# Kernel optimization log

Hardware: AMD Instinct MI355X
Metric: run time of the kernel (lower is better)

Reference implementation:

```python
import jax, jax.numpy as jnp
import numpy as np

H = 24        # attn.heads (Flux)
ENC = 512     # encoder (text) token count, hard-coded in the source via emb[:512]
EPS = 1e-6    # RMSNorm eps


def _rms(x, w):
    # RMSNorm over head_dim (Flux norm_q / norm_k)
    return x * jax.lax.rsqrt(jnp.mean(x * x, axis=-1, keepdims=True) + EPS) * w


def _rope(x, cos, sin):
    # diffusers apply_rotary_emb, use_real=True, unbind_dim=-1
    xr = x.reshape(x.shape[:-1] + (-1, 2))
    rot = jnp.stack([-xr[..., 1], xr[..., 0]], axis=-1).reshape(x.shape)
    return x * cos + rot * sin


def setup_inputs() -> dict:
    key = jax.random.key(0)
    ks = jax.random.split(key, 26)
    B, F, D = 2, 1024, 3072
    hd = D // H
    S = ENC + F
    lin = lambda k: 0.02 * jax.random.normal(k, (D, D), jnp.float32)
    bias = lambda k: 0.02 * jax.random.normal(k, (D,), jnp.float32)
    nw = lambda k: 1.0 + 0.02 * jax.random.normal(k, (hd,), jnp.float32)
    return {
        'hidden_states': jax.random.normal(ks[0], (B, F, D), jnp.float32),
        'encoder_hidden_states': jax.random.normal(ks[1], (B, ENC, D), jnp.float32),
        'rot_cos': jax.random.uniform(ks[2], (S, hd), jnp.float32, minval=-1.0, maxval=1.0),
        'rot_sin': jax.random.uniform(ks[3], (S, hd), jnp.float32, minval=-1.0, maxval=1.0),
        'wq': lin(ks[4]), 'bq': bias(ks[5]),
        'wk': lin(ks[6]), 'bk': bias(ks[7]),
        'wv': lin(ks[8]), 'bv': bias(ks[9]),
        'waq': lin(ks[10]), 'baq': bias(ks[11]),
        'wak': lin(ks[12]), 'bak': bias(ks[13]),
        'wav': lin(ks[14]), 'bav': bias(ks[15]),
        'wo': lin(ks[16]), 'bo': bias(ks[17]),
        'wao': lin(ks[18]), 'bao': bias(ks[19]),
        'nq': nw(ks[20]), 'nk': nw(ks[21]),
        'naq': nw(ks[22]), 'nak': nw(ks[23]),
    }


def reference(hidden_states, encoder_hidden_states, rot_cos, rot_sin,
              wq, bq, wk, bk, wv, bv, waq, baq, wak, bak, wav, bav,
              wo, bo, wao, bao, nq, nk, naq, nak):
    B, F, D = hidden_states.shape
    hd = D // H

    def proj(x, w, b):
        y = x @ w.T + b
        return y.reshape(x.shape[0], -1, H, hd).transpose(0, 2, 1, 3)  # [B,H,S,hd]

    q = _rms(proj(hidden_states, wq, bq), nq)   # [B,H,F,hd]
    k = _rms(proj(hidden_states, wk, bk), nk)
    v = proj(hidden_states, wv, bv)

    # cross-batch mixing: 'b h f d -> 1 h (b f) d' then repeat over batch
    k = jnp.broadcast_to(k.transpose(1, 0, 2, 3).reshape(1, H, B * F, hd), (B, H, B * F, hd))
    v = jnp.broadcast_to(v.transpose(1, 0, 2, 3).reshape(1, H, B * F, hd), (B, H, B * F, hd))

    # key rotary: encoder part once, image part repeated num_components times
    cos_k = jnp.concatenate([rot_cos[:ENC]] + [rot_cos[ENC:]] * B, axis=0)
    sin_k = jnp.concatenate([rot_sin[:ENC]] + [rot_sin[ENC:]] * B, axis=0)

    eq = _rms(proj(encoder_hidden_states, waq, baq), naq)  # [B,H,ENC,hd]
    ek = _rms(proj(encoder_hidden_states, wak, bak), nak)
    ev = proj(encoder_hidden_states, wav, bav)

    q = jnp.concatenate([eq, q], axis=2)  # [B,H,ENC+F,hd]
    k = jnp.concatenate([ek, k], axis=2)  # [B,H,ENC+B*F,hd]
    v = jnp.concatenate([ev, v], axis=2)

    q = _rope(q, rot_cos, rot_sin)
    k = _rope(k, cos_k, sin_k)

    scale = hd ** -0.5
    attn = jax.nn.softmax(jnp.einsum('bhqd,bhkd->bhqk', q, k) * scale, axis=-1)
    out = jnp.einsum('bhqk,bhkd->bhqd', attn, v)
    out = out.transpose(0, 2, 1, 3).reshape(B, -1, D)  # [B,ENC+F,D]

    enc_out = out[:, :ENC] @ wao.T + bao
    hs_out = out[:, ENC:] @ wo.T + bo
    return (hs_out, enc_out)
```

## Files before the change

### kernel.cpp

```cpp
#include <hip/hip_runtime.h>

typedef __attribute__((ext_vector_type(8))) short bf16x8;
typedef __attribute__((ext_vector_type(8))) unsigned short u16x8;
typedef __attribute__((ext_vector_type(4))) unsigned short u16x4;
typedef __attribute__((ext_vector_type(4))) float f32x4;
typedef __attribute__((ext_vector_type(2))) unsigned uint2v;

#define DEV static __device__ __forceinline__

DEV unsigned short f2bf(float f){
  unsigned u = __float_as_uint(f);
  u += 0x7fff + ((u>>16)&1);
  return (unsigned short)(u>>16);
}
DEV float bf2f(unsigned short b){ return __uint_as_float(((unsigned)b)<<16); }
DEV unsigned cvtpk(float lo, float hi){
  unsigned r;
  asm("v_cvt_pk_bf16_f32 %0, %1, %2" : "=v"(r) : "v"(lo), "v"(hi));
  return r;
}

DEV void gll16(const void* g, void* l){
  __builtin_amdgcn_global_load_lds((__attribute__((address_space(1))) unsigned*)(void*)g,
                                   (__attribute__((address_space(3))) unsigned*)l, 16, 0, 0);
}

__global__ void k_cast(const float* __restrict__ x, unsigned short* __restrict__ y, int n4){
  int i = blockIdx.x*256 + threadIdx.x;
  if (i >= n4) return;
  f32x4 v = ((const f32x4*)x)[i];
  u16x4 o = { f2bf(v.x), f2bf(v.y), f2bf(v.z), f2bf(v.w) };
  ((u16x4*)y)[i] = o;
}

__global__ void k_castW(const float* __restrict__ s0, const float* __restrict__ s1,
                        const float* __restrict__ s2, const float* __restrict__ s3,
                        const float* __restrict__ s4, const float* __restrict__ s5,
                        unsigned short* __restrict__ y){
  unsigned i = blockIdx.x*256 + threadIdx.x;
  unsigned seg = i / 2359296u;
  unsigned off = i - seg*2359296u;
  const float* s = seg==0?s0: seg==1?s1: seg==2?s2: seg==3?s3: seg==4?s4: s5;
  f32x4 v = ((const f32x4*)s)[off];
  u16x4 o = { f2bf(v.x), f2bf(v.y), f2bf(v.z), f2bf(v.w) };
  ((u16x4*)y)[i] = o;
}

__global__ __launch_bounds__(256) void k_gemmP(
    const unsigned short* __restrict__ X, const unsigned short* __restrict__ W,
    unsigned short* __restrict__ Y,
    const float* __restrict__ b0, const float* __restrict__ b1, const float* __restrict__ b2)
{
  const int K = 3072, N = 9216;
  __shared__ unsigned short As[2][4096];
  __shared__ unsigned short Bs[2][4096];
  const int t = threadIdx.x, w = t>>6, l = t&63;
  const int by = blockIdx.y, bx = blockIdx.x;
  const int sec = by>=48 ? 2 : (by>=24 ? 1 : 0);
  const int Cl = (by - sec*24)*128;
  const int R = bx*128;
  const unsigned short* Wp = W + (long)sec*9437184 + (long)Cl*K;
  const float* bias = (sec==0)?b0:(sec==1)?b1:b2;
  const int wr = w>>1, wc = w&1;
  f32x4 acc[4][4] = {};

  auto stage = [&](int buf, int kt){
    const int k0 = kt*32;
    #pragma unroll
    for (int c=0;c<2;c++){
      int row = c*64 + (t>>2);
      int scol = ((t&3)<<3) ^ ((row&3)<<3);
      gll16(X + (long)(R+row)*K + k0 + scol, &As[buf][c*2048 + w*512]);
      gll16(Wp + (long)row*K + k0 + scol, &Bs[buf][c*2048 + w*512]);
    }
  };

  stage(0,0);
  int buf = 0;
  for (int kt=0; kt<96; kt++){
    __syncthreads();
    if (kt+1 < 96) stage(buf^1, kt+1);
    bf16x8 a[4], b[4];
    #pragma unroll
    for (int m=0;m<4;m++){
      int ar = wr*64 + m*16 + (l&15);
      int ac = ((l>>4)<<3) ^ ((ar&3)<<3);
      a[m] = *(const bf16x8*)&As[buf][ar*32 + ac];
      int br = wc*64 + m*16 + (l&15);
      int bc2 = ((l>>4)<<3) ^ ((br&3)<<3);
      b[m] = *(const bf16x8*)&Bs[buf][br*32 + bc2];
    }
    #pragma unroll
    for (int m=0;m<4;m++)
      #pragma unroll
      for (int n=0;n<4;n++)
        acc[m][n] = __builtin_amdgcn_mfma_f32_16x16x32_bf16(a[m], b[n], acc[m][n], 0,0,0);
    buf ^= 1;
  }

  #pragma unroll
  for (int m=0;m<4;m++){
    int row = R + wr*64 + m*16 + ((l>>4)<<2);
    #pragma unroll
    for (int n=0;n<4;n++){
      int cl = wc*64 + n*16 + (l&15);
      float bvv = bias[Cl + cl];
      long col = (long)by*128 + cl;
      #pragma unroll
      for (int r=0;r<4;r++)
        Y[(long)(row+r)*N + col] = f2bf(acc[m][n][r] + bvv);
    }
  }
}

__global__ __launch_bounds__(256) void k_gemmO(
    const unsigned short* __restrict__ X, const unsigned short* __restrict__ Wf,
    float* __restrict__ out, const float* __restrict__ bo, const float* __restrict__ bao)
{
  const int K = 3072;
  __shared__ unsigned short As[2][4096];
  __shared__ unsigned short Bs[2][4096];
  const int t = threadIdx.x, w = t>>6, l = t&63;
  const int bx = blockIdx.x, by = blockIdx.y;
  const bool enc = bx >= 16;
  const unsigned short* Wp = Wf + (enc ? 9437184 : 0);
  const float* bias = enc ? bao : bo;
  const int R = bx*128, C = by*128;
  long xbase, obase;
  if (!enc){ xbase = (long)(R>>10)*1536 + 512 + (R&1023); obase = (long)R*3072; }
  else { int Rp = R-2048; xbase = (long)(Rp>>9)*1536 + (Rp&511); obase = 6291456 + (long)Rp*3072; }
  const int wr = w>>1, wc = w&1;
  f32x4 acc[4][4] = {};

  auto stage = [&](int buf, int kt){
    const int k0 = kt*32;
    #pragma unroll
    for (int c=0;c<2;c++){
      int row = c*64 + (t>>2);
      int scol = ((t&3)<<3) ^ ((row&3)<<3);
      gll16(X + (xbase+row)*K + k0 + scol, &As[buf][c*2048 + w*512]);
      gll16(Wp + (long)(C+row)*K + k0 + scol, &Bs[buf][c*2048 + w*512]);
    }
  };

  stage(0,0);
  int buf = 0;
  for (int kt=0; kt<96; kt++){
    __syncthreads();
    if (kt+1 < 96) stage(buf^1, kt+1);
    bf16x8 a[4], b[4];
    #pragma unroll
    for (int m=0;m<4;m++){
      int ar = wr*64 + m*16 + (l&15);
      int ac = ((l>>4)<<3) ^ ((ar&3)<<3);
      a[m] = *(const bf16x8*)&As[buf][ar*32 + ac];
      int br = wc*64 + m*16 + (l&15);
      int bc2 = ((l>>4)<<3) ^ ((br&3)<<3);
      b[m] = *(const bf16x8*)&Bs[buf][br*32 + bc2];
    }
    #pragma unroll
    for (int m=0;m<4;m++)
      #pragma unroll
      for (int n=0;n<4;n++)
        acc[m][n] = __builtin_amdgcn_mfma_f32_16x16x32_bf16(a[m], b[n], acc[m][n], 0,0,0);
    buf ^= 1;
  }

  #pragma unroll
  for (int m=0;m<4;m++){
    int rl = wr*64 + m*16 + ((l>>4)<<2);
    #pragma unroll
    for (int n=0;n<4;n++){
      int col = C + wc*64 + n*16 + (l&15);
      float bvv = bias[col];
      #pragma unroll
      for (int r=0;r<4;r++)
        out[obase + (long)(rl+r)*3072 + col] = acc[m][n][r] + bvv;
    }
  }
}

__global__ void k_ppqk(const unsigned short* __restrict__ Y, int ystr, int yoff,
    const float* __restrict__ nw,
    const float* __restrict__ cs, const float* __restrict__ sn, unsigned short* __restrict__ dst,
    int T_log2, int tpb_log2, int dest_off, int S, int no_batch,
    int pos_off, int pos_mask, float qscale)
{
  int rid = blockIdx.x*4 + (threadIdx.x>>6);
  int l = threadIdx.x & 63;
  int h = rid >> T_log2, tk = rid & ((1<<T_log2)-1);
  unsigned pair = *(const unsigned*)(Y + (long)tk*ystr + yoff + h*128 + 2*l);
  float x0 = bf2f((unsigned short)(pair&0xffff));
  float x1 = bf2f((unsigned short)(pair>>16));
  float ss = x0*x0 + x1*x1;
  #pragma unroll
  for (int m=1;m<64;m<<=1) ss += __shfl_xor(ss, m);
  float rr = rsqrtf(ss*(1.0f/128.0f) + 1e-6f);
  x0 *= rr*nw[2*l]; x1 *= rr*nw[2*l+1];
  int p = pos_off + (tk & pos_mask);
  float c0 = cs[p*128 + 2*l], c1 = cs[p*128 + 2*l+1];
  float s0 = sn[p*128 + 2*l], s1 = sn[p*128 + 2*l+1];
  float o0 = (x0*c0 - x1*s0)*qscale;
  float o1 = (x1*c1 + x0*s1)*qscale;
  long idx;
  if (no_batch) idx = (long)h*S + tk;
  else {
    int b = tk >> tpb_log2;
    int sq = dest_off + (tk & ((1<<tpb_log2)-1));
    idx = (long)(b*24+h)*S + sq;
  }
  unsigned out = (unsigned)f2bf(o0) | ((unsigned)f2bf(o1)<<16);
  *(unsigned*)(dst + idx*128 + 2*l) = out;
}

__global__ void k_ppv(const unsigned short* __restrict__ Y, int ystr, int yoff,
                      unsigned short* __restrict__ Vt, int vstr, int no_batch)
{
  __shared__ unsigned short tileS[64][136];
  int t = threadIdx.x, h = blockIdx.y;
  int tile0 = blockIdx.x*64;
  #pragma unroll
  for (int c=0;c<4;c++){
    int j = c*16 + (t>>4), col = (t&15)*8;
    *(u16x8*)&tileS[j][col] = *(const u16x8*)(Y + (long)(tile0+j)*ystr + yoff + h*128 + col);
  }
  __syncthreads();
  int d = t>>1, half = t&1;
  unsigned short tmp[32];
  #pragma unroll
  for (int i=0;i<32;i++) tmp[i] = tileS[half*32+i][d];
  long base;
  if (no_batch) base = ((long)h*128 + d)*vstr + tile0 + half*32;
  else { int b = tile0>>9; base = ((long)(b*24+h)*128 + d)*vstr + (tile0&511) + half*32; }
  #pragma unroll
  for (int k=0;k<4;k++) *(u16x8*)(Vt + base + k*8) = *(const u16x8*)&tmp[k*8];
}

__global__ __launch_bounds__(256) void k_attn(
    const unsigned short* __restrict__ Q,
    const unsigned short* __restrict__ Ke, const unsigned short* __restrict__ Ki,
    const unsigned short* __restrict__ Ve, const unsigned short* __restrict__ Vi,
    unsigned short* __restrict__ AO)
{
  __shared__ unsigned short Ks[8192];
  __shared__ unsigned short Vs[8192];
  __shared__ unsigned short Ps[4][1408];
  const int t = threadIdx.x, w = t>>6, l = t&63;
  const int h = blockIdx.y, b = blockIdx.z;
  const int bh = b*24 + h;
  const int q0 = blockIdx.x*64 + w*16;
  const int g = l>>4;

  auto stageK = [&](int jt){
    const unsigned short* ksrc = (jt < 8) ? Ke + ((long)bh*512 + jt*64)*128
                                          : Ki + ((long)h*2048 + (jt-8)*64)*128;
    #pragma unroll
    for (int c=0;c<4;c++){
      int row = c*16 + (t>>4);
      int col = ((t&15)<<3) ^ ((row&7)<<3);
      gll16(ksrc + row*128 + col, &Ks[c*2048 + w*512]);
    }
  };
  auto stageV = [&](int jt){
    const unsigned short* vsrc; long vstr;
    if (jt < 8){ vsrc = Ve + (long)bh*65536 + jt*64; vstr = 512; }
    else { vsrc = Vi + (long)h*262144 + (jt-8)*64; vstr = 2048; }
    #pragma unroll
    for (int c=0;c<4;c++){
      int row = c*32 + (t>>3);
      int col = ((t&7)<<3) ^ ((row&7)<<3);
      gll16(vsrc + (long)row*vstr + col, &Vs[c*2048 + w*512]);
    }
  };

  bf16x8 qf[4];
  {
    const unsigned short* qp = Q + ((long)bh*1536 + q0 + (l&15))*128 + (g<<3);
    #pragma unroll
    for (int kc=0;kc<4;kc++) qf[kc] = *(const bf16x8*)(qp + kc*32);
  }
  f32x4 o[8] = {};
  float mx = -1e30f;
  float ls = 0.f;

  stageK(0);
  for (int jt=0; jt<40; jt++){
    __syncthreads();
    stageV(jt);

    f32x4 sf[4];
    __builtin_amdgcn_s_setprio(1);
    #pragma unroll
    for (int ct=0;ct<4;ct++){
      f32x4 s = {};
      #pragma unroll
      for (int kc=0;kc<4;kc++){
        int krow = ct*16 + (l&15);
        int kcol = (kc*32 + (g<<3)) ^ ((krow&7)<<3);
        bf16x8 kb = *(const bf16x8*)&Ks[krow*128 + kcol];
        s = __builtin_amdgcn_mfma_f32_16x16x32_bf16(kb, qf[kc], s, 0,0,0);
      }
      sf[ct] = s;
    }
    __builtin_amdgcn_s_setprio(0);

    float pm = sf[0][0];
    #pragma unroll
    for (int ct=0;ct<4;ct++)
      #pragma unroll
      for (int r=0;r<4;r++) pm = fmaxf(pm, sf[ct][r]);
    if (!__all(pm <= mx + 8.0f)){
      float tmax = pm;
      tmax = fmaxf(tmax, __shfl_xor(tmax, 16));
      tmax = fmaxf(tmax, __shfl_xor(tmax, 32));
      float mn = fmaxf(mx, tmax);
      float al = exp2f(mx - mn);
      mx = mn;
      ls *= al;
      #pragma unroll
      for (int r=0;r<4;r++){
        float alo = __shfl(al, (l&48) | ((g<<2)+r));
        #pragma unroll
        for (int f=0;f<8;f++) o[f][r] *= alo;
      }
    }
    #pragma unroll
    for (int ct=0;ct<4;ct++){
      float p0 = exp2f(sf[ct][0]-mx), p1 = exp2f(sf[ct][1]-mx);
      float p2 = exp2f(sf[ct][2]-mx), p3 = exp2f(sf[ct][3]-mx);
      ls += (p0+p1)+(p2+p3);
      uint2v pk = { cvtpk(p0,p1), cvtpk(p2,p3) };
      *(uint2v*)&Ps[w][(l&15)*88 + ct*16 + (g<<2)] = pk;
    }
    __syncthreads();

    if (jt+1 < 40) stageK(jt+1);

    bf16x8 pa[2];
    #pragma unroll
    for (int kc=0;kc<2;kc++)
      pa[kc] = *(const bf16x8*)&Ps[w][(l&15)*88 + kc*32 + (g<<3)];
    __builtin_amdgcn_s_setprio(1);
    #pragma unroll
    for (int f=0;f<8;f++){
      #pragma unroll
      for (int kc=0;kc<2;kc++){
        int vrow = f*16 + (l&15);
        int vcol = (kc*32 + (g<<3)) ^ ((vrow&7)<<3);
        bf16x8 vb = *(const bf16x8*)&Vs[vrow*64 + vcol];
        o[f] = __builtin_amdgcn_mfma_f32_16x16x32_bf16(pa[kc], vb, o[f], 0,0,0);
      }
    }
    __builtin_amdgcn_s_setprio(0);
  }

  ls += __shfl_xor(ls, 16);
  ls += __shfl_xor(ls, 32);
  #pragma unroll
  for (int r=0;r<4;r++){
    float lso = __shfl(ls, (l&48) | ((g<<2)+r));
    float inv = 1.0f/lso;
    int qrow = q0 + (g<<2) + r;
    #pragma unroll
    for (int f=0;f<8;f++){
      AO[((long)b*1536 + qrow)*3072 + h*128 + f*16 + (l&15)] = f2bf(o[f][r]*inv);
    }
  }
}

extern "C" void kernel_launch(void* const* d_in, const int* in_sizes, int n_in,
                              void* d_out, int out_size, void* d_ws, size_t ws_size,
                              hipStream_t stream)
{
  const float* hs  = (const float*)d_in[0];
  const float* ehs = (const float*)d_in[1];
  const float* rc  = (const float*)d_in[2];
  const float* rs_ = (const float*)d_in[3];
  const float* wq = (const float*)d_in[4];  const float* bq = (const float*)d_in[5];
  const float* wk = (const float*)d_in[6];  const float* bk = (const float*)d_in[7];
  const float* wv = (const float*)d_in[8];  const float* bv = (const float*)d_in[9];
  const float* waq= (const float*)d_in[10]; const float* baq= (const float*)d_in[11];
  const float* wak= (const float*)d_in[12]; const float* bak= (const float*)d_in[13];
  const float* wav= (const float*)d_in[14]; const float* bav= (const float*)d_in[15];
  const float* wo = (const float*)d_in[16]; const float* bo = (const float*)d_in[17];
  const float* wao= (const float*)d_in[18]; const float* bao= (const float*)d_in[19];
  const float* nq = (const float*)d_in[20]; const float* nk = (const float*)d_in[21];
  const float* naq= (const float*)d_in[22]; const float* nak= (const float*)d_in[23];

  const float qsc = (float)(0.08838834764831845 * 1.4426950408889634);

  char* p = (char*)d_ws;
  auto alloc = [&](size_t bytes){ char* r = p; p += bytes; return r; };

  if (ws_size >= (size_t)245366784){
    unsigned short* Xh = (unsigned short*)alloc(12582912);
    unsigned short* Xe = (unsigned short*)alloc(6291456);
    unsigned short* Wb = (unsigned short*)alloc(113246208);
    unsigned short* Yb = (unsigned short*)alloc(56623104);
    unsigned short* Qb = (unsigned short*)alloc(18874368);
    unsigned short* Ke = (unsigned short*)alloc(6291456);
    unsigned short* Ki = (unsigned short*)alloc(12582912);
    unsigned short* Ve = (unsigned short*)alloc(6291456);
    unsigned short* Vi = (unsigned short*)alloc(12582912);
    unsigned short* AO = Xh;
    unsigned short* Ye = Yb + (long)18874368;

    k_cast<<<6144,256,0,stream>>>(hs, Xh, 1572864);
    k_cast<<<3072,256,0,stream>>>(ehs, Xe, 786432);
    k_castW<<<55296,256,0,stream>>>(wq, wk, wv, waq, wak, wav, Wb);

    k_gemmP<<<dim3(16,72),256,0,stream>>>(Xh, Wb, Yb, bq, bk, bv);
    k_gemmP<<<dim3(8,72),256,0,stream>>>(Xe, Wb + 28311552, Ye, baq, bak, bav);

    k_ppqk<<<12288,256,0,stream>>>(Yb, 9216, 0,    nq,  rc, rs_, Qb, 11, 10, 512, 1536, 0, 512, 1023, qsc);
    k_ppqk<<<12288,256,0,stream>>>(Yb, 9216, 3072, nk,  rc, rs_, Ki, 11, 0,  0,   2048, 1, 512, 1023, 1.0f);
    k_ppv<<<dim3(32,24),256,0,stream>>>(Yb, 9216, 6144, Vi, 2048, 1);
    k_ppqk<<<6144,256,0,stream>>>(Ye, 9216, 0,    naq, rc, rs_, Qb, 10, 9, 0, 1536, 0, 0, 511, qsc);
    k_ppqk<<<6144,256,0,stream>>>(Ye, 9216, 3072, nak, rc, rs_, Ke, 10, 9, 0, 512,  0, 0, 511, 1.0f);
    k_ppv<<<dim3(16,24),256,0,stream>>>(Ye, 9216, 6144, Ve, 512, 0);

    k_attn<<<dim3(24,24,2),256,0,stream>>>(Qb, Ke, Ki, Ve, Vi, AO);

    k_cast<<<9216,256,0,stream>>>(wo,  Wb, 2359296);
    k_cast<<<9216,256,0,stream>>>(wao, Wb + 9437184, 2359296);
    k_gemmO<<<dim3(24,24),256,0,stream>>>(AO, Wb, (float*)d_out, bo, bao);
  } else {
    unsigned short* Xh = (unsigned short*)alloc(12582912);
    unsigned short* Xe = (unsigned short*)alloc(6291456);
    unsigned short* Wb = (unsigned short*)alloc(56623104);
    unsigned short* Yb = (unsigned short*)alloc(37748736);
    unsigned short* Qb = (unsigned short*)alloc(18874368);
    unsigned short* Ke = (unsigned short*)alloc(6291456);
    unsigned short* Ki = (unsigned short*)alloc(12582912);
    unsigned short* Ve = (unsigned short*)alloc(6291456);
    unsigned short* Vi = (unsigned short*)alloc(12582912);
    unsigned short* AO = Xh;

    k_cast<<<6144,256,0,stream>>>(hs, Xh, 1572864);
    k_cast<<<3072,256,0,stream>>>(ehs, Xe, 786432);

    k_cast<<<9216,256,0,stream>>>(wq, Wb, 2359296);
    k_cast<<<9216,256,0,stream>>>(wk, Wb + 9437184, 2359296);
    k_cast<<<9216,256,0,stream>>>(wv, Wb + 18874368, 2359296);
    k_gemmP<<<dim3(16,72),256,0,stream>>>(Xh, Wb, Yb, bq, bk, bv);
    k_ppqk<<<12288,256,0,stream>>>(Yb, 9216, 0,    nq, rc, rs_, Qb, 11, 10, 512, 1536, 0, 512, 1023, qsc);
    k_ppqk<<<12288,256,0,stream>>>(Yb, 9216, 3072, nk, rc, rs_, Ki, 11, 0,  0,   2048, 1, 512, 1023, 1.0f);
    k_ppv<<<dim3(32,24),256,0,stream>>>(Yb, 9216, 6144, Vi, 2048, 1);

    k_cast<<<9216,256,0,stream>>>(waq, Wb, 2359296);
    k_cast<<<9216,256,0,stream>>>(wak, Wb + 9437184, 2359296);
    k_cast<<<9216,256,0,stream>>>(wav, Wb + 18874368, 2359296);
    k_gemmP<<<dim3(8,72),256,0,stream>>>(Xe, Wb, Yb, baq, bak, bav);
    k_ppqk<<<6144,256,0,stream>>>(Yb, 9216, 0,    naq, rc, rs_, Qb, 10, 9, 0, 1536, 0, 0, 511, qsc);
    k_ppqk<<<6144,256,0,stream>>>(Yb, 9216, 3072, nak, rc, rs_, Ke, 10, 9, 0, 512,  0, 0, 511, 1.0f);
    k_ppv<<<dim3(16,24),256,0,stream>>>(Yb, 9216, 6144, Ve, 512, 0);

    k_attn<<<dim3(24,24,2),256,0,stream>>>(Qb, Ke, Ki, Ve, Vi, AO);

    k_cast<<<9216,256,0,stream>>>(wo,  Wb, 2359296);
    k_cast<<<9216,256,0,stream>>>(wao, Wb + 9437184, 2359296);
    k_gemmO<<<dim3(24,24),256,0,stream>>>(AO, Wb, (float*)d_out, bo, bao);
  }
}
```

Baseline: 709.3 us.

## Fuse RMSNorm and RoPE into projection GEMM epilogue; double-buffer attention K/V

The QKV projection GEMM now applies bias, RMSNorm (a cross-wave row reduction through shared memory), RoPE and the query scale directly in its epilogue for the Q and K sections. It writes Q and K straight into their attention layouts, so the separate k_ppqk passes and the bf16 round trip through Y are removed. Separately, the attention kernel now double-buffers K and V tiles, prefetching the next tile at the top of each iteration, and drops one barrier per iteration. The trade-offs are extra shuffles and scattered 2-byte stores in the GEMM epilogue, and twice the shared memory in attention, which may lower occupancy.

```diff
diff --git a/kernel.cpp b/kernel.cpp
--- a/kernel.cpp
+++ b/kernel.cpp
@@ -49,15 +49,22 @@
 __global__ __launch_bounds__(256) void k_gemmP(
     const unsigned short* __restrict__ X, const unsigned short* __restrict__ W,
     unsigned short* __restrict__ Y,
-    const float* __restrict__ b0, const float* __restrict__ b1, const float* __restrict__ b2)
+    const float* __restrict__ b0, const float* __restrict__ b1, const float* __restrict__ b2,
+    const float* __restrict__ nqw, const float* __restrict__ nkw,
+    const float* __restrict__ cs, const float* __restrict__ sn,
+    unsigned short* __restrict__ Qd, unsigned short* __restrict__ Kd,
+    int is_img)
 {
   const int K = 3072, N = 9216;
-  __shared__ unsigned short As[2][4096];
-  __shared__ unsigned short Bs[2][4096];
+  __shared__ unsigned short SH[17408];
+  unsigned short (*As)[4096] = (unsigned short(*)[4096])SH;
+  unsigned short (*Bs)[4096] = (unsigned short(*)[4096])(SH + 8192);
   const int t = threadIdx.x, w = t>>6, l = t&63;
+  const int li = l&15, g = l>>4;
   const int by = blockIdx.y, bx = blockIdx.x;
   const int sec = by>=48 ? 2 : (by>=24 ? 1 : 0);
-  const int Cl = (by - sec*24)*128;
+  const int hd = by - sec*24;
+  const int Cl = hd*128;
   const int R = bx*128;
   const unsigned short* Wp = W + (long)sec*9437184 + (long)Cl*K;
   const float* bias = (sec==0)?b0:(sec==1)?b1:b2;
@@ -83,11 +90,11 @@
     bf16x8 a[4], b[4];
     #pragma unroll
     for (int m=0;m<4;m++){
-      int ar = wr*64 + m*16 + (l&15);
-      int ac = ((l>>4)<<3) ^ ((ar&3)<<3);
+      int ar = wr*64 + m*16 + li;
+      int ac = (g<<3) ^ ((ar&3)<<3);
       a[m] = *(const bf16x8*)&As[buf][ar*32 + ac];
-      int br = wc*64 + m*16 + (l&15);
-      int bc2 = ((l>>4)<<3) ^ ((br&3)<<3);
+      int br = wc*64 + m*16 + li;
+      int bc2 = (g<<3) ^ ((br&3)<<3);
       b[m] = *(const bf16x8*)&Bs[buf][br*32 + bc2];
     }
     #pragma unroll
@@ -98,17 +105,93 @@
     buf ^= 1;
   }
 
+  float bias_n[4];
+  #pragma unroll
+  for (int n=0;n<4;n++) bias_n[n] = bias[Cl + wc*64 + n*16 + li];
+
+  if (sec == 2){
+    #pragma unroll
+    for (int m=0;m<4;m++){
+      int row = R + wr*64 + m*16 + (g<<2);
+      #pragma unroll
+      for (int n=0;n<4;n++){
+        long col = (long)by*128 + wc*64 + n*16 + li;
+        #pragma unroll
+        for (int r=0;r<4;r++)
+          Y[(long)(row+r)*N + col] = f2bf(acc[m][n][r] + bias_n[n]);
+      }
+    }
+    return;
+  }
+
+  float part[4][4];
+  #pragma unroll
+  for (int m=0;m<4;m++)
+    #pragma unroll
+    for (int r=0;r<4;r++){
+      float s_ = 0.f;
+      #pragma unroll
+      for (int n=0;n<4;n++){ float v = acc[m][n][r] + bias_n[n]; s_ += v*v; }
+      part[m][r] = s_;
+    }
+  #pragma unroll
+  for (int m=0;m<4;m++)
+    #pragma unroll
+    for (int r=0;r<4;r++){
+      part[m][r] += __shfl_xor(part[m][r], 1);
+      part[m][r] += __shfl_xor(part[m][r], 2);
+      part[m][r] += __shfl_xor(part[m][r], 4);
+      part[m][r] += __shfl_xor(part[m][r], 8);
+    }
+  __syncthreads();
+  float* rs = (float*)SH;
+  if (li == 0){
+    #pragma unroll
+    for (int m=0;m<4;m++)
+      #pragma unroll
+      for (int r=0;r<4;r++)
+        rs[(wc*2+wr)*64 + m*16 + g*4 + r] = part[m][r];
+  }
+  __syncthreads();
+  float fac[4][4];
+  #pragma unroll
+  for (int m=0;m<4;m++)
+    #pragma unroll
+    for (int r=0;r<4;r++){
+      int idx = m*16 + g*4 + r;
+      float tot = rs[(0*2+wr)*64 + idx] + rs[(1*2+wr)*64 + idx];
+      fac[m][r] = rsqrtf(tot*(1.0f/128.0f) + 1e-6f);
+    }
+
+  const float* nw = (sec==0) ? nqw : nkw;
+  const float qs = (sec==0) ? (float)(0.08838834764831845 * 1.4426950408889634) : 1.0f;
+  float nw_n[4];
+  #pragma unroll
+  for (int n=0;n<4;n++) nw_n[n] = nw[wc*64 + n*16 + li];
+
   #pragma unroll
   for (int m=0;m<4;m++){
-    int row = R + wr*64 + m*16 + ((l>>4)<<2);
-    #pragma unroll
-    for (int n=0;n<4;n++){
-      int cl = wc*64 + n*16 + (l&15);
-      float bvv = bias[Cl + cl];
-      long col = (long)by*128 + cl;
-      #pragma unroll
-      for (int r=0;r<4;r++)
-        Y[(long)(row+r)*N + col] = f2bf(acc[m][n][r] + bvv);
+    #pragma unroll
+    for (int r=0;r<4;r++){
+      int row_l = wr*64 + m*16 + g*4 + r;
+      int t_row = R + row_l;
+      int b_, s_, p_;
+      if (is_img){ b_ = t_row>>10; s_ = t_row&1023; p_ = 512+s_; }
+      else       { b_ = t_row>>9;  s_ = t_row&511;  p_ = s_; }
+      long didx;
+      if (sec==0) didx = (long)(b_*24+hd)*1536 + (is_img ? 512+s_ : s_);
+      else        didx = is_img ? ((long)hd*2048 + t_row) : ((long)(b_*24+hd)*512 + s_);
+      const float* crow = cs + (long)p_*128;
+      const float* srow = sn + (long)p_*128;
+      unsigned short* drow = ((sec==0)?Qd:Kd) + didx*128;
+      #pragma unroll
+      for (int n=0;n<4;n++){
+        int cl = wc*64 + n*16 + li;
+        float x = (acc[m][n][r] + bias_n[n]) * fac[m][r] * nw_n[n];
+        float xo = __shfl_xor(x, 1);
+        float o_ = x*crow[cl] + ((l&1) ? xo*srow[cl] : -xo*srow[cl]);
+        drow[cl] = f2bf(o_*qs);
+      }
     }
   }
 }
@@ -180,39 +263,6 @@
   }
 }
 
-__global__ void k_ppqk(const unsigned short* __restrict__ Y, int ystr, int yoff,
-    const float* __restrict__ nw,
-    const float* __restrict__ cs, const float* __restrict__ sn, unsigned short* __restrict__ dst,
-    int T_log2, int tpb_log2, int dest_off, int S, int no_batch,
-    int pos_off, int pos_mask, float qscale)
-{
-  int rid = blockIdx.x*4 + (threadIdx.x>>6);
-  int l = threadIdx.x & 63;
-  int h = rid >> T_log2, tk = rid & ((1<<T_log2)-1);
-  unsigned pair = *(const unsigned*)(Y + (long)tk*ystr + yoff + h*128 + 2*l);
-  float x0 = bf2f((unsigned short)(pair&0xffff));
-  float x1 = bf2f((unsigned short)(pair>>16));
-  float ss = x0*x0 + x1*x1;
-  #pragma unroll
-  for (int m=1;m<64;m<<=1) ss += __shfl_xor(ss, m);
-  float rr = rsqrtf(ss*(1.0f/128.0f) + 1e-6f);
-  x0 *= rr*nw[2*l]; x1 *= rr*nw[2*l+1];
-  int p = pos_off + (tk & pos_mask);
-  float c0 = cs[p*128 + 2*l], c1 = cs[p*128 + 2*l+1];
-  float s0 = sn[p*128 + 2*l], s1 = sn[p*128 + 2*l+1];
-  float o0 = (x0*c0 - x1*s0)*qscale;
-  float o1 = (x1*c1 + x0*s1)*qscale;
-  long idx;
-  if (no_batch) idx = (long)h*S + tk;
-  else {
-    int b = tk >> tpb_log2;
-    int sq = dest_off + (tk & ((1<<tpb_log2)-1));
-    idx = (long)(b*24+h)*S + sq;
-  }
-  unsigned out = (unsigned)f2bf(o0) | ((unsigned)f2bf(o1)<<16);
-  *(unsigned*)(dst + idx*128 + 2*l) = out;
-}
-
 __global__ void k_ppv(const unsigned short* __restrict__ Y, int ystr, int yoff,
                       unsigned short* __restrict__ Vt, int vstr, int no_batch)
 {
@@ -242,8 +292,8 @@
     const unsigned short* __restrict__ Ve, const unsigned short* __restrict__ Vi,
     unsigned short* __restrict__ AO)
 {
-  __shared__ unsigned short Ks[8192];
-  __shared__ unsigned short Vs[8192];
+  __shared__ unsigned short Ks[2][8192];
+  __shared__ unsigned short Vs[2][8192];
   __shared__ unsigned short Ps[4][1408];
   const int t = threadIdx.x, w = t>>6, l = t&63;
   const int h = blockIdx.y, b = blockIdx.z;
@@ -251,17 +301,17 @@
   const int q0 = blockIdx.x*64 + w*16;
   const int g = l>>4;
 
-  auto stageK = [&](int jt){
+  auto stageK = [&](int jt, int bufi){
     const unsigned short* ksrc = (jt < 8) ? Ke + ((long)bh*512 + jt*64)*128
                                           : Ki + ((long)h*2048 + (jt-8)*64)*128;
     #pragma unroll
     for (int c=0;c<4;c++){
       int row = c*16 + (t>>4);
       int col = ((t&15)<<3) ^ ((row&7)<<3);
-      gll16(ksrc + row*128 + col, &Ks[c*2048 + w*512]);
+      gll16(ksrc + row*128 + col, &Ks[bufi][c*2048 + w*512]);
     }
   };
-  auto stageV = [&](int jt){
+  auto stageV = [&](int jt, int bufi){
     const unsigned short* vsrc; long vstr;
     if (jt < 8){ vsrc = Ve + (long)bh*65536 + jt*64; vstr = 512; }
     else { vsrc = Vi + (long)h*262144 + (jt-8)*64; vstr = 2048; }
@@ -269,7 +319,7 @@
     for (int c=0;c<4;c++){
       int row = c*32 + (t>>3);
       int col = ((t&7)<<3) ^ ((row&7)<<3);
-      gll16(vsrc + (long)row*vstr + col, &Vs[c*2048 + w*512]);
+      gll16(vsrc + (long)row*vstr + col, &Vs[bufi][c*2048 + w*512]);
     }
   };
 
@@ -283,10 +333,11 @@
   float mx = -1e30f;
   float ls = 0.f;
 
-  stageK(0);
+  stageK(0,0); stageV(0,0);
+  int buf = 0;
   for (int jt=0; jt<40; jt++){
     __syncthreads();
-    stageV(jt);
+    if (jt+1 < 40){ stageK(jt+1, buf^1); stageV(jt+1, buf^1); }
 
     f32x4 sf[4];
     __builtin_amdgcn_s_setprio(1);
@@ -297,7 +348,7 @@
       for (int kc=0;kc<4;kc++){
         int krow = ct*16 + (l&15);
         int kcol = (kc*32 + (g<<3)) ^ ((krow&7)<<3);
-        bf16x8 kb = *(const bf16x8*)&Ks[krow*128 + kcol];
+        bf16x8 kb = *(const bf16x8*)&Ks[buf][krow*128 + kcol];
         s = __builtin_amdgcn_mfma_f32_16x16x32_bf16(kb, qf[kc], s, 0,0,0);
       }
       sf[ct] = s;
@@ -332,9 +383,7 @@
       uint2v pk = { cvtpk(p0,p1), cvtpk(p2,p3) };
       *(uint2v*)&Ps[w][(l&15)*88 + ct*16 + (g<<2)] = pk;
     }
-    __syncthreads();
-
-    if (jt+1 < 40) stageK(jt+1);
+    asm volatile("" ::: "memory");
 
     bf16x8 pa[2];
     #pragma unroll
@@ -347,11 +396,12 @@
       for (int kc=0;kc<2;kc++){
         int vrow = f*16 + (l&15);
         int vcol = (kc*32 + (g<<3)) ^ ((vrow&7)<<3);
-        bf16x8 vb = *(const bf16x8*)&Vs[vrow*64 + vcol];
+        bf16x8 vb = *(const bf16x8*)&Vs[buf][vrow*64 + vcol];
         o[f] = __builtin_amdgcn_mfma_f32_16x16x32_bf16(pa[kc], vb, o[f], 0,0,0);
       }
     }
     __builtin_amdgcn_s_setprio(0);
+    buf ^= 1;
   }
 
   ls += __shfl_xor(ls, 16);
@@ -387,8 +437,6 @@
   const float* nq = (const float*)d_in[20]; const float* nk = (const float*)d_in[21];
   const float* naq= (const float*)d_in[22]; const float* nak= (const float*)d_in[23];
 
-  const float qsc = (float)(0.08838834764831845 * 1.4426950408889634);
-
   char* p = (char*)d_ws;
   auto alloc = [&](size_t bytes){ char* r = p; p += bytes; return r; };
 
@@ -409,14 +457,12 @@
     k_cast<<<3072,256,0,stream>>>(ehs, Xe, 786432);
     k_castW<<<55296,256,0,stream>>>(wq, wk, wv, waq, wak, wav, Wb);
 
-    k_gemmP<<<dim3(16,72),256,0,stream>>>(Xh, Wb, Yb, bq, bk, bv);
-    k_gemmP<<<dim3(8,72),256,0,stream>>>(Xe, Wb + 28311552, Ye, baq, bak, bav);
-
-    k_ppqk<<<12288,256,0,stream>>>(Yb, 9216, 0,    nq,  rc, rs_, Qb, 11, 10, 512, 1536, 0, 512, 1023, qsc);
-    k_ppqk<<<12288,256,0,stream>>>(Yb, 9216, 3072, nk,  rc, rs_, Ki, 11, 0,  0,   2048, 1, 512, 1023, 1.0f);
+    k_gemmP<<<dim3(16,72),256,0,stream>>>(Xh, Wb, Yb, bq, bk, bv,
+                                          nq, nk, rc, rs_, Qb, Ki, 1);
+    k_gemmP<<<dim3(8,72),256,0,stream>>>(Xe, Wb + 28311552, Ye, baq, bak, bav,
+                                         naq, nak, rc, rs_, Qb, Ke, 0);
+
     k_ppv<<<dim3(32,24),256,0,stream>>>(Yb, 9216, 6144, Vi, 2048, 1);
-    k_ppqk<<<6144,256,0,stream>>>(Ye, 9216, 0,    naq, rc, rs_, Qb, 10, 9, 0, 1536, 0, 0, 511, qsc);
-    k_ppqk<<<6144,256,0,stream>>>(Ye, 9216, 3072, nak, rc, rs_, Ke, 10, 9, 0, 512,  0, 0, 511, 1.0f);
     k_ppv<<<dim3(16,24),256,0,stream>>>(Ye, 9216, 6144, Ve, 512, 0);
 
     k_attn<<<dim3(24,24,2),256,0,stream>>>(Qb, Ke, Ki, Ve, Vi, AO);
@@ -442,17 +488,15 @@
     k_cast<<<9216,256,0,stream>>>(wq, Wb, 2359296);
     k_cast<<<9216,256,0,stream>>>(wk, Wb + 9437184, 2359296);
     k_cast<<<9216,256,0,stream>>>(wv, Wb + 18874368, 2359296);
-    k_gemmP<<<dim3(16,72),256,0,stream>>>(Xh, Wb, Yb, bq, bk, bv);
-    k_ppqk<<<12288,256,0,stream>>>(Yb, 9216, 0,    nq, rc, rs_, Qb, 11, 10, 512, 1536, 0, 512, 1023, qsc);
-    k_ppqk<<<12288,256,0,stream>>>(Yb, 9216, 3072, nk, rc, rs_, Ki, 11, 0,  0,   2048, 1, 512, 1023, 1.0f);
+    k_gemmP<<<dim3(16,72),256,0,stream>>>(Xh, Wb, Yb, bq, bk, bv,
+                                          nq, nk, rc, rs_, Qb, Ki, 1);
     k_ppv<<<dim3(32,24),256,0,stream>>>(Yb, 9216, 6144, Vi, 2048, 1);
 
     k_cast<<<9216,256,0,stream>>>(waq, Wb, 2359296);
     k_cast<<<9216,256,0,stream>>>(wak, Wb + 9437184, 2359296);
     k_cast<<<9216,256,0,stream>>>(wav, Wb + 18874368, 2359296);
-    k_gemmP<<<dim3(8,72),256,0,stream>>>(Xe, Wb, Yb, baq, bak, bav);
-    k_ppqk<<<6144,256,0,stream>>>(Yb, 9216, 0,    naq, rc, rs_, Qb, 10, 9, 0, 1536, 0, 0, 511, qsc);
-    k_ppqk<<<6144,256,0,stream>>>(Yb, 9216, 3072, nak, rc, rs_, Ke, 10, 9, 0, 512,  0, 0, 511, 1.0f);
+    k_gemmP<<<dim3(8,72),256,0,stream>>>(Xe, Wb, Yb, baq, bak, bav,
+                                         naq, nak, rc, rs_, Qb, Ke, 0);
     k_ppv<<<dim3(16,24),256,0,stream>>>(Yb, 9216, 6144, Ve, 512, 0);
 
     k_attn<<<dim3(24,24,2),256,0,stream>>>(Qb, Ke, Ki, Ve, Vi, AO);
```

After: 742.6 us. 4.7% more time.
